# Kernel tuning notes

Hardware: AMD Instinct MI355X
Metric: run time of the kernel (lower is better)

Reference implementation:

```python
import jax, jax.numpy as jnp
import numpy as np

N, K, D = 131072, 1024, 10


def setup_inputs() -> dict:
    key = jax.random.key(0)
    k1, k2 = jax.random.split(key)
    encoder_embedding = jax.random.normal(k1, (N, D), dtype=jnp.float32)
    embedding_weight = jax.random.normal(k2, (K, D), dtype=jnp.float32)
    return {"encoder_embedding": encoder_embedding, "embedding_weight": embedding_weight}


def reference(encoder_embedding, embedding_weight):
    x = encoder_embedding            # [N, D]
    E = embedding_weight             # [K, D]
    x_sq = jnp.sum(x * x, axis=1, keepdims=True)          # [N, 1]
    e_sq = jnp.sum(E * E, axis=1)                         # [K]
    distance = x_sq + e_sq - 2.0 * jnp.einsum('nd,kd->nk', x, E)
    idx = jnp.argmin(distance, axis=1)                    # [N]
    quantized = E[idx]                                    # [N, D] gather
    # codebook (quantization) loss: mse(x.detach(), quantized)
    diff = jax.lax.stop_gradient(x) - quantized
    quantization_loss = jnp.mean(diff * diff)
    # straight-through estimator
    quantized_st = x + jax.lax.stop_gradient(quantized - x)
    return (quantized_st, quantization_loss)
```

## Files before the change

### kernel.cpp

```cpp
#include <hip/hip_runtime.h>


typedef __attribute__((ext_vector_type(8))) short short8;
typedef __attribute__((ext_vector_type(16))) float f32x16;

constexpr int N = 131072;
constexpr int K = 1024;
constexpr int D = 10;
constexpr int TILES = 32;
constexpr int THREADS = 512;
constexpr int BLOCKS = 512;
constexpr int GROUPS = 8;
constexpr int RPG = 32;
constexpr int TPW = 4;
constexpr int AFRAG_N = TILES * 3 * 64;

__device__ float4 g_afrag[AFRAG_N];

__device__ inline unsigned short f2bf(float f) {
    unsigned u = __float_as_uint(f);
    u += 0x7FFFu + ((u >> 16) & 1u);
    return (unsigned short)(u >> 16);
}
__device__ inline float bf2f(unsigned short h) {
    return __uint_as_float(((unsigned)h) << 16);
}

__global__ __launch_bounds__(256) void prep_afrag(const float* __restrict__ E) {
    const int gid = blockIdx.x * blockDim.x + threadIdx.x;
    if (gid >= AFRAG_N) return;
    const int tile = gid / 192;
    const int rem  = gid % 192;
    const int v    = rem / 64;
    const int L    = rem % 64;
    const int code = tile * 32 + (L & 31);
    const int h    = L >> 5;

    float e[D];
    #pragma unroll
    for (int d = 0; d < D; ++d) e[d] = E[code * D + d];
    float s = 0.f;
    #pragma unroll
    for (int d = 0; d < D; ++d) s = fmaf(e[d], e[d], s);
    const float ms = -0.5f * s;
    const unsigned short msh = f2bf(ms);
    const float r1 = ms - bf2f(msh);
    const unsigned short msm = f2bf(r1);
    const unsigned short msl = f2bf(r1 - bf2f(msm));

    unsigned short sl[8];
    #pragma unroll
    for (int i = 0; i < 8; ++i) {
        const int k = h * 8 + i;
        unsigned short o = 0;
        if (k < D) {
            const unsigned short eh = f2bf(e[k]);
            if (v == 0) o = eh;
            else {
                const float rm = e[k] - bf2f(eh);
                const unsigned short em = f2bf(rm);
                o = (v == 1) ? em : f2bf(rm - bf2f(em));
            }
        } else if (v == 0) {
            o = (k == 10) ? msh : (k == 11) ? msm : (k == 12) ? msl : (unsigned short)0;
        }
        sl[i] = o;
    }
    float4 w;
    unsigned* wp = (unsigned*)&w;
    #pragma unroll
    for (int q = 0; q < 4; ++q)
        wp[q] = (unsigned)sl[2 * q] | ((unsigned)sl[2 * q + 1] << 16);
    g_afrag[gid] = w;
}

__device__ inline void build_b_row(const float* __restrict__ x, int grow,
                                   int row, short8* __restrict__ sB) {
    const float* xp = x + (size_t)grow * D;
    float xv[D];
    #pragma unroll
    for (int d = 0; d < D; d += 2) {
        float2 t2 = *reinterpret_cast<const float2*>(xp + d);
        xv[d] = t2.x; xv[d + 1] = t2.y;
    }
    unsigned short XH[D], XM[D], XL[D];
    #pragma unroll
    for (int d = 0; d < D; ++d) {
        XH[d] = f2bf(xv[d]); const float r1 = xv[d] - bf2f(XH[d]);
        XM[d] = f2bf(r1);    XL[d] = f2bf(r1 - bf2f(XM[d]));
    }
    unsigned short slots[48];
    #pragma unroll
    for (int s = 0; s < 16; ++s) {
        slots[s]      = (s < D) ? XH[s]
                      : (s <= 12 ? (unsigned short)0x3F80 : (unsigned short)0);
        slots[16 + s] = (s < D) ? XM[s] : (unsigned short)0;
        slots[32 + s] = (s < D) ? XL[s] : (unsigned short)0;
    }
    #pragma unroll
    for (int v = 0; v < 3; ++v)
        #pragma unroll
        for (int h = 0; h < 2; ++h) {
            short8 w;
            #pragma unroll
            for (int i = 0; i < 8; ++i) w[i] = (short)slots[v * 16 + h * 8 + i];
            sB[(v * 2 + h) * 32 + row] = w;
        }
}

#define MFMA __builtin_amdgcn_mfma_f32_32x32x16_bf16

__global__ __launch_bounds__(THREADS, 4) void vq_kernel(
    const float* __restrict__ x,
    const float* __restrict__ E,
    float* __restrict__ out,
    float* __restrict__ loss_out)
{
    __shared__ short8 sB[6 * 32];
    __shared__ float  sScore[8][RPG];
    __shared__ int    sIdx[8][RPG];

    const int tid  = threadIdx.x;
    const int lane = tid & 63;
    const int wave = tid >> 6;
    const int n    = lane & 31;
    const int hf   = lane >> 5;
    const int hibase = hf * 4;
    const int wtile  = wave * TPW;
    const int blockRow = blockIdx.x * (GROUPS * RPG);

    const short8* ga = (const short8*)g_afrag;
    short8 a[TPW][3];
    #pragma unroll
    for (int t = 0; t < TPW; ++t)
        #pragma unroll
        for (int v = 0; v < 3; ++v)
            a[t][v] = ga[((wtile + t) * 3 + v) * 64 + lane];

    if (tid < RPG) build_b_row(x, blockRow + tid, tid, sB);
    __syncthreads();

    float lsum = 0.f;

    for (int g = 0; g < GROUPS; ++g) {
        const int rowBase = blockRow + g * RPG;

        const short8 b0 = sB[(0 * 2 + hf) * 32 + n];
        const short8 b1 = sB[(1 * 2 + hf) * 32 + n];
        const short8 b2 = sB[(2 * 2 + hf) * 32 + n];

        float best = -3.0e38f;
        int   lci  = 0;

        #pragma unroll
        for (int p = 0; p < TPW / 2; ++p) {
            const int t0 = 2 * p, t1 = 2 * p + 1;
            f32x16 c0, c1;
            #pragma unroll
            for (int i = 0; i < 16; ++i) { c0[i] = 0.f; c1[i] = 0.f; }
            c0 = MFMA(a[t0][0], b0, c0, 0, 0, 0);  c1 = MFMA(a[t1][0], b0, c1, 0, 0, 0);
            c0 = MFMA(a[t0][0], b1, c0, 0, 0, 0);  c1 = MFMA(a[t1][0], b1, c1, 0, 0, 0);
            c0 = MFMA(a[t0][0], b2, c0, 0, 0, 0);  c1 = MFMA(a[t1][0], b2, c1, 0, 0, 0);
            c0 = MFMA(a[t0][1], b0, c0, 0, 0, 0);  c1 = MFMA(a[t1][1], b0, c1, 0, 0, 0);
            c0 = MFMA(a[t0][1], b1, c0, 0, 0, 0);  c1 = MFMA(a[t1][1], b1, c1, 0, 0, 0);
            c0 = MFMA(a[t0][2], b0, c0, 0, 0, 0);  c1 = MFMA(a[t1][2], b0, c1, 0, 0, 0);

            #pragma unroll
            for (int r = 0; r < 16; ++r) {
                const bool gt = c0[r] > best;
                lci  = gt ? (t0 * 16 + r) : lci;
                best = fmaxf(best, c0[r]);
            }
            #pragma unroll
            for (int r = 0; r < 16; ++r) {
                const bool gt = c1[r] > best;
                lci  = gt ? (t1 * 16 + r) : lci;
                best = fmaxf(best, c1[r]);
            }
        }

        const int tt = lci >> 4, rr = lci & 15;
        int bidx = (wtile + tt) * 32 + hibase + ((rr & 3) + 8 * (rr >> 2));

        {
            const float pb = __shfl_xor(best, 32, 64);
            const int   pi = __shfl_xor(bidx, 32, 64);
            const bool take = (pb > best) || (pb == best && pi < bidx);
            best = take ? pb : best;  bidx = take ? pi : bidx;
        }
        if (lane < 32) { sScore[wave][n] = best; sIdx[wave][n] = bidx; }
        __syncthreads();

        if (tid < RPG) {
            float bs = sScore[0][tid];
            int   bi = sIdx[0][tid];
            #pragma unroll
            for (int w = 1; w < 8; ++w) {
                const float s  = sScore[w][tid];
                const int   i2 = sIdx[w][tid];
                if (s > bs) { bs = s; bi = i2; }
            }
            const float* ep = E   + (size_t)bi * D;
            const float* xp = x   + (size_t)(rowBase + tid) * D;
            float*       op = out + (size_t)(rowBase + tid) * D;
            #pragma unroll
            for (int d = 0; d < D; d += 2) {
                float2 ev = *reinterpret_cast<const float2*>(ep + d);
                float2 xw = *reinterpret_cast<const float2*>(xp + d);
                const float d0 = xw.x - ev.x, d1 = xw.y - ev.y;
                lsum = fmaf(d0, d0, lsum);  lsum = fmaf(d1, d1, lsum);
                float2 o;
                o.x = xw.x + (ev.x - xw.x);
                o.y = xw.y + (ev.y - xw.y);
                *reinterpret_cast<float2*>(op + d) = o;
            }
            if (g + 1 < GROUPS)
                build_b_row(x, rowBase + RPG + tid, tid, sB);
        }
        __syncthreads();
    }

    if (tid < 64) {
        #pragma unroll
        for (int off = 32; off > 0; off >>= 1)
            lsum += __shfl_down(lsum, off, 64);
        if (tid == 0)
            atomicAdd(loss_out, lsum * (1.0f / ((float)N * (float)D)));
    }
}

extern "C" void kernel_launch(void* const* d_in, const int* in_sizes, int n_in,
                              void* d_out, int out_size, void* d_ws, size_t ws_size,
                              hipStream_t stream) {
    const float* x = (const float*)d_in[0];
    const float* E = (const float*)d_in[1];
    float* out  = (float*)d_out;
    float* loss = out + (size_t)N * D;

    hipMemsetAsync(loss, 0, sizeof(float), stream);
    prep_afrag<<<dim3(AFRAG_N / 256), dim3(256), 0, stream>>>(E);
    vq_kernel<<<dim3(BLOCKS), dim3(THREADS), 0, stream>>>(x, E, out, loss);
}
```

Baseline: 93.49 us.

## Fuse codebook prep into VQ kernel and batch all row groups per block

Drops the separate prep kernel: each wave now builds its bf16 triple-split codebook fragments in registers straight from E, removing a launch and a global round-trip. The B fragments for all 8 row groups are staged into shared memory at once, and per-group argmin results are stored with 16-bit indices. This replaces the two block barriers per group with one barrier before a single final reduction, gather and write pass over 256 rows. The cost is more shared memory and redundant codebook conversion in every block.

```diff
diff --git a/kernel.cpp b/kernel.cpp
--- a/kernel.cpp
+++ b/kernel.cpp
@@ -7,15 +7,12 @@
 constexpr int N = 131072;
 constexpr int K = 1024;
 constexpr int D = 10;
-constexpr int TILES = 32;
 constexpr int THREADS = 512;
 constexpr int BLOCKS = 512;
+constexpr int RPB = 256;
 constexpr int GROUPS = 8;
 constexpr int RPG = 32;
 constexpr int TPW = 4;
-constexpr int AFRAG_N = TILES * 3 * 64;
-
-__device__ float4 g_afrag[AFRAG_N];
 
 __device__ inline unsigned short f2bf(float f) {
     unsigned u = __float_as_uint(f);
@@ -26,56 +23,8 @@
     return __uint_as_float(((unsigned)h) << 16);
 }
 
-__global__ __launch_bounds__(256) void prep_afrag(const float* __restrict__ E) {
-    const int gid = blockIdx.x * blockDim.x + threadIdx.x;
-    if (gid >= AFRAG_N) return;
-    const int tile = gid / 192;
-    const int rem  = gid % 192;
-    const int v    = rem / 64;
-    const int L    = rem % 64;
-    const int code = tile * 32 + (L & 31);
-    const int h    = L >> 5;
-
-    float e[D];
-    #pragma unroll
-    for (int d = 0; d < D; ++d) e[d] = E[code * D + d];
-    float s = 0.f;
-    #pragma unroll
-    for (int d = 0; d < D; ++d) s = fmaf(e[d], e[d], s);
-    const float ms = -0.5f * s;
-    const unsigned short msh = f2bf(ms);
-    const float r1 = ms - bf2f(msh);
-    const unsigned short msm = f2bf(r1);
-    const unsigned short msl = f2bf(r1 - bf2f(msm));
-
-    unsigned short sl[8];
-    #pragma unroll
-    for (int i = 0; i < 8; ++i) {
-        const int k = h * 8 + i;
-        unsigned short o = 0;
-        if (k < D) {
-            const unsigned short eh = f2bf(e[k]);
-            if (v == 0) o = eh;
-            else {
-                const float rm = e[k] - bf2f(eh);
-                const unsigned short em = f2bf(rm);
-                o = (v == 1) ? em : f2bf(rm - bf2f(em));
-            }
-        } else if (v == 0) {
-            o = (k == 10) ? msh : (k == 11) ? msm : (k == 12) ? msl : (unsigned short)0;
-        }
-        sl[i] = o;
-    }
-    float4 w;
-    unsigned* wp = (unsigned*)&w;
-    #pragma unroll
-    for (int q = 0; q < 4; ++q)
-        wp[q] = (unsigned)sl[2 * q] | ((unsigned)sl[2 * q + 1] << 16);
-    g_afrag[gid] = w;
-}
-
 __device__ inline void build_b_row(const float* __restrict__ x, int grow,
-                                   int row, short8* __restrict__ sB) {
+                                   int g, int row, short8* __restrict__ sB) {
     const float* xp = x + (size_t)grow * D;
     float xv[D];
     #pragma unroll
@@ -104,7 +53,7 @@
             short8 w;
             #pragma unroll
             for (int i = 0; i < 8; ++i) w[i] = (short)slots[v * 16 + h * 8 + i];
-            sB[(v * 2 + h) * 32 + row] = w;
+            sB[(g * 6 + v * 2 + h) * 32 + row] = w;
         }
 }
 
@@ -116,9 +65,9 @@
     float* __restrict__ out,
     float* __restrict__ loss_out)
 {
-    __shared__ short8 sB[6 * 32];
-    __shared__ float  sScore[8][RPG];
-    __shared__ int    sIdx[8][RPG];
+    __shared__ short8 sB[GROUPS * 6 * 32];
+    __shared__ float  sScore[8][RPB];
+    __shared__ unsigned short sIdxs[8][RPB];
 
     const int tid  = threadIdx.x;
     const int lane = tid & 63;
@@ -127,27 +76,60 @@
     const int hf   = lane >> 5;
     const int hibase = hf * 4;
     const int wtile  = wave * TPW;
-    const int blockRow = blockIdx.x * (GROUPS * RPG);
-
-    const short8* ga = (const short8*)g_afrag;
+    const int blockRow = blockIdx.x * RPB;
+
     short8 a[TPW][3];
     #pragma unroll
-    for (int t = 0; t < TPW; ++t)
-        #pragma unroll
-        for (int v = 0; v < 3; ++v)
-            a[t][v] = ga[((wtile + t) * 3 + v) * 64 + lane];
-
-    if (tid < RPG) build_b_row(x, blockRow + tid, tid, sB);
+    for (int t = 0; t < TPW; ++t) {
+        const int code = (wtile + t) * 32 + n;
+        const float* ep = E + (size_t)code * D;
+        float e[D];
+        #pragma unroll
+        for (int d = 0; d < D; d += 2) {
+            float2 t2 = *reinterpret_cast<const float2*>(ep + d);
+            e[d] = t2.x; e[d + 1] = t2.y;
+        }
+        float s = 0.f;
+        #pragma unroll
+        for (int d = 0; d < D; ++d) s = fmaf(e[d], e[d], s);
+        const float ms = -0.5f * s;
+        const unsigned short msh = f2bf(ms);
+        const float r1 = ms - bf2f(msh);
+        const unsigned short msm = f2bf(r1);
+        const unsigned short msl = f2bf(r1 - bf2f(msm));
+
+        #pragma unroll
+        for (int v = 0; v < 3; ++v) {
+            short8 w;
+            #pragma unroll
+            for (int i = 0; i < 8; ++i) {
+                const int k = hf * 8 + i;
+                unsigned short o = 0;
+                if (k < D) {
+                    const unsigned short eh = f2bf(e[k]);
+                    if (v == 0) o = eh;
+                    else {
+                        const float rm = e[k] - bf2f(eh);
+                        const unsigned short em = f2bf(rm);
+                        o = (v == 1) ? em : f2bf(rm - bf2f(em));
+                    }
+                } else if (v == 0) {
+                    o = (k == 10) ? msh : (k == 11) ? msm
+                      : (k == 12) ? msl : (unsigned short)0;
+                }
+                w[i] = (short)o;
+            }
+            a[t][v] = w;
+        }
+    }
+
+    if (tid < RPB) build_b_row(x, blockRow + tid, tid >> 5, tid & 31, sB);
     __syncthreads();
 
-    float lsum = 0.f;
-
     for (int g = 0; g < GROUPS; ++g) {
-        const int rowBase = blockRow + g * RPG;
-
-        const short8 b0 = sB[(0 * 2 + hf) * 32 + n];
-        const short8 b1 = sB[(1 * 2 + hf) * 32 + n];
-        const short8 b2 = sB[(2 * 2 + hf) * 32 + n];
+        const short8 b0 = sB[(g * 6 + 0 + hf) * 32 + n];
+        const short8 b1 = sB[(g * 6 + 2 + hf) * 32 + n];
+        const short8 b2 = sB[(g * 6 + 4 + hf) * 32 + n];
 
         float best = -3.0e38f;
         int   lci  = 0;
@@ -188,45 +170,44 @@
             const bool take = (pb > best) || (pb == best && pi < bidx);
             best = take ? pb : best;  bidx = take ? pi : bidx;
         }
-        if (lane < 32) { sScore[wave][n] = best; sIdx[wave][n] = bidx; }
-        __syncthreads();
-
-        if (tid < RPG) {
-            float bs = sScore[0][tid];
-            int   bi = sIdx[0][tid];
-            #pragma unroll
-            for (int w = 1; w < 8; ++w) {
-                const float s  = sScore[w][tid];
-                const int   i2 = sIdx[w][tid];
-                if (s > bs) { bs = s; bi = i2; }
-            }
-            const float* ep = E   + (size_t)bi * D;
-            const float* xp = x   + (size_t)(rowBase + tid) * D;
-            float*       op = out + (size_t)(rowBase + tid) * D;
-            #pragma unroll
-            for (int d = 0; d < D; d += 2) {
-                float2 ev = *reinterpret_cast<const float2*>(ep + d);
-                float2 xw = *reinterpret_cast<const float2*>(xp + d);
-                const float d0 = xw.x - ev.x, d1 = xw.y - ev.y;
-                lsum = fmaf(d0, d0, lsum);  lsum = fmaf(d1, d1, lsum);
-                float2 o;
-                o.x = xw.x + (ev.x - xw.x);
-                o.y = xw.y + (ev.y - xw.y);
-                *reinterpret_cast<float2*>(op + d) = o;
-            }
-            if (g + 1 < GROUPS)
-                build_b_row(x, rowBase + RPG + tid, tid, sB);
-        }
-        __syncthreads();
-    }
-
-    if (tid < 64) {
-        #pragma unroll
-        for (int off = 32; off > 0; off >>= 1)
-            lsum += __shfl_down(lsum, off, 64);
-        if (tid == 0)
-            atomicAdd(loss_out, lsum * (1.0f / ((float)N * (float)D)));
-    }
+        if (lane < 32) {
+            sScore[wave][g * RPG + n] = best;
+            sIdxs[wave][g * RPG + n]  = (unsigned short)bidx;
+        }
+    }
+    __syncthreads();
+
+    float lsum = 0.f;
+    if (tid < RPB) {
+        float bs = sScore[0][tid];
+        int   bi = sIdxs[0][tid];
+        #pragma unroll
+        for (int w = 1; w < 8; ++w) {
+            const float s  = sScore[w][tid];
+            const int   i2 = sIdxs[w][tid];
+            if (s > bs) { bs = s; bi = i2; }
+        }
+        const float* ep = E   + (size_t)bi * D;
+        const float* xp = x   + (size_t)(blockRow + tid) * D;
+        float*       op = out + (size_t)(blockRow + tid) * D;
+        #pragma unroll
+        for (int d = 0; d < D; d += 2) {
+            float2 ev = *reinterpret_cast<const float2*>(ep + d);
+            float2 xw = *reinterpret_cast<const float2*>(xp + d);
+            const float d0 = xw.x - ev.x, d1 = xw.y - ev.y;
+            lsum = fmaf(d0, d0, lsum);  lsum = fmaf(d1, d1, lsum);
+            float2 o;
+            o.x = xw.x + (ev.x - xw.x);
+            o.y = xw.y + (ev.y - xw.y);
+            *reinterpret_cast<float2*>(op + d) = o;
+        }
+    }
+
+    #pragma unroll
+    for (int off = 32; off > 0; off >>= 1)
+        lsum += __shfl_down(lsum, off, 64);
+    if (lane == 0)
+        atomicAdd(loss_out, lsum * (1.0f / ((float)N * (float)D)));
 }
 
 extern "C" void kernel_launch(void* const* d_in, const int* in_sizes, int n_in,
@@ -238,6 +219,5 @@
     float* loss = out + (size_t)N * D;
 
     hipMemsetAsync(loss, 0, sizeof(float), stream);
-    prep_afrag<<<dim3(AFRAG_N / 256), dim3(256), 0, stream>>>(E);
     vq_kernel<<<dim3(BLOCKS), dim3(THREADS), 0, stream>>>(x, E, out, loss);
 }
```

Result: slower. 135.6 us (+45.0%).
